# Optimization experiments

Measured on AMD Instinct MI355X. Metric: run time of the kernel, lower is better.

## Reference

```python
import jax, jax.numpy as jnp
import numpy as np

NEG_SLOPE = 0.2
N, E, NNZ, IN, H, C = 100000, 50000, 800000, 128, 8, 16


def setup_inputs() -> dict:
    key = jax.random.key(0)
    ks = jax.random.split(key, 8)
    X = jax.random.normal(ks[0], (N, IN), jnp.float32)
    W_typed = jax.random.normal(ks[1], (4, IN, H * C), jnp.float32) * (1.0 / np.sqrt(IN))
    att_e = jax.random.normal(ks[2], (4, H, C), jnp.float32) * 0.1
    att_v = jax.random.normal(ks[3], (4, H, C), jnp.float32) * 0.1
    vertex = jax.random.randint(ks[4], (NNZ,), 0, N, jnp.int32)
    edges = jax.random.randint(ks[5], (NNZ,), 0, E, jnp.int32)
    vtype = jax.random.randint(ks[6], (N,), 0, 4, jnp.int32)
    etype = jax.random.randint(ks[7], (E,), 0, 4, jnp.int32)
    return {"X": X, "W_typed": W_typed, "att_e": att_e, "att_v": att_v,
            "vertex": vertex, "edges": edges, "vtype": vtype, "etype": etype}


def _segment_softmax(logits, seg, num):
    # numerically-stable softmax over segments (PyG-style, eps in denominator)
    m = jax.ops.segment_max(logits, seg, num_segments=num)
    ex = jnp.exp(logits - m[seg])
    s = jax.ops.segment_sum(ex, seg, num_segments=num)
    return ex / (s[seg] + 1e-16)


def reference(X, W_typed, att_e, att_v, vertex, edges, vtype, etype):
    # typed linear: project with all 4 type weights, select per node type
    Xall = jnp.einsum('ni,tio->tno', X, W_typed)        # [4, N, H*C]
    X0 = Xall[vtype, jnp.arange(N)]                     # [N, H*C]
    Xn = X0.reshape(N, H, C)
    Xve = Xn[vertex]                                    # [NNZ, H, C] gather vertex->incidence
    # vertex->edge attention, typed by edge type of each incidence
    beta = jnp.sum(Xve * att_e[etype[edges]], axis=-1)  # [NNZ, H]
    beta = jax.nn.leaky_relu(beta, NEG_SLOPE)
    beta = _segment_softmax(beta, edges, E)
    Xe = jax.nn.relu(jax.ops.segment_sum(Xve * beta[..., None], edges, num_segments=E))  # [E, H, C]
    Xe = Xe[edges]                                      # [NNZ, H, C] gather edge->incidence
    # edge->vertex attention, typed by node type of each incidence's vertex
    alpha = jnp.sum(Xe * att_v[vtype[vertex]], axis=-1)  # [NNZ, H]
    alpha = jax.nn.leaky_relu(alpha, NEG_SLOPE)
    alpha = _segment_softmax(alpha, vertex, N)
    Xv = jax.ops.segment_sum(Xe * alpha[..., None], vertex, num_segments=N)  # [N, H, C]
    return Xv.reshape(N, H * C)
```

## Files before the change

### kernel.cpp

```cpp
#include <hip/hip_runtime.h>

typedef __attribute__((ext_vector_type(8))) short bf16x8;
typedef __attribute__((ext_vector_type(4))) float f32x4;

#define NEG_SLOPE 0.2f

__device__ __forceinline__ unsigned short f2bf(float f){
  unsigned u = __float_as_uint(f);
  u = (u + 0x7fffu + ((u >> 16) & 1u)) >> 16;
  return (unsigned short)u;
}
__device__ __forceinline__ float bflo(unsigned u){ return __uint_as_float(u << 16); }
__device__ __forceinline__ float bfhi(unsigned u){ return __uint_as_float(u & 0xffff0000u); }

__global__ __launch_bounds__(256) void k_histprep(
    const int* __restrict__ edges, const int* __restrict__ vertex, int NNZ,
    int* __restrict__ cnt, int E, int nbHist,
    const int* __restrict__ vtype, int N, int* __restrict__ tcnt, int nbHN,
    const float* __restrict__ W, short* __restrict__ Bfrag){
  __shared__ int lcnt[4];
  int b = (int)blockIdx.x;
  if (b < nbHist){
    int i = b * 256 + threadIdx.x;
    if (i < NNZ){
      atomicAdd(cnt + edges[i], 1);
      atomicAdd(cnt + E + vertex[i], 1);
    }
    return;
  }
  b -= nbHist;
  if (b < nbHN){
    if (threadIdx.x < 4) lcnt[threadIdx.x] = 0;
    __syncthreads();
    int i = b * 256 + threadIdx.x;
    if (i < N) atomicAdd(&lcnt[vtype[i]], 1);
    __syncthreads();
    if (threadIdx.x < 4 && lcnt[threadIdx.x] > 0)
      atomicAdd(tcnt + threadIdx.x, lcnt[threadIdx.x]);
    return;
  }
  b -= nbHN;
  int u = b * 256 + threadIdx.x;
  int j = u & 7, lane = (u >> 3) & 63, ct = (u >> 9) & 31, ks = u >> 14;
  int k = ks * 32 + ((lane >> 4) << 3) + j;
  int col = (ct << 4) + (lane & 15);
  int t = col >> 7, o = col & 127;
  Bfrag[u] = (short)f2bf(W[(t * 128 + k) * 128 + o]);
}

__global__ __launch_bounds__(256) void k_scanA(const int* __restrict__ cnt, int S,
                                               int* __restrict__ bsum){
  __shared__ int sh[256];
  int base = blockIdx.x * 1024 + threadIdx.x * 4;
  int s = 0;
  #pragma unroll
  for (int k = 0; k < 4; ++k){ int idx = base + k; if (idx < S) s += cnt[idx]; }
  sh[threadIdx.x] = s; __syncthreads();
  for (int off = 128; off > 0; off >>= 1){
    if (threadIdx.x < off) sh[threadIdx.x] += sh[threadIdx.x + off];
    __syncthreads();
  }
  if (threadIdx.x == 0) bsum[blockIdx.x] = sh[0];
}

__global__ void k_scanB(int* bsum, int nb, const int* __restrict__ tcnt,
                        int* __restrict__ pbase){
  if (threadIdx.x == 0 && blockIdx.x == 0){
    int run = 0;
    for (int b = 0; b < nb; ++b){ int v = bsum[b]; bsum[b] = run; run += v; }
    int pb = 0;
    for (int t = 0; t < 4; ++t){
      pbase[t] = pb;
      pb += ((tcnt[t] + 63) >> 6) << 6;
    }
    pbase[4] = pb;
  }
}

__global__ __launch_bounds__(256) void k_scanC(const int* __restrict__ cnt, int S,
    const int* __restrict__ bsum, int* __restrict__ offs, int* __restrict__ cursor,
    int nbS, const int* __restrict__ vtype, int N, const int* __restrict__ pbase,
    int* __restrict__ tcur, int* __restrict__ nsorted){
  __shared__ int sh[256];
  __shared__ int gbase[4];
  int t = threadIdx.x;
  int b = (int)blockIdx.x;
  if (b >= nbS){
    int* lcnt = sh;
    if (t < 4) lcnt[t] = 0;
    __syncthreads();
    int i = (b - nbS) * 256 + t;
    int tt = 0, rank = 0;
    bool valid = i < N;
    if (valid){ tt = vtype[i]; rank = atomicAdd(&lcnt[tt], 1); }
    __syncthreads();
    if (t < 4 && lcnt[t] > 0) gbase[t] = atomicAdd(tcur + t, lcnt[t]);
    __syncthreads();
    if (valid) nsorted[pbase[tt] + gbase[tt] + rank] = i;
    return;
  }
  int base = b * 1024 + t * 4;
  int c[4]; int s = 0;
  #pragma unroll
  for (int k = 0; k < 4; ++k){ int idx = base + k; c[k] = (idx < S) ? cnt[idx] : 0; s += c[k]; }
  sh[t] = s; __syncthreads();
  for (int off = 1; off < 256; off <<= 1){
    int v = (t >= off) ? sh[t - off] : 0; __syncthreads();
    sh[t] += v; __syncthreads();
  }
  int run = bsum[b] + sh[t] - s;
  #pragma unroll
  for (int k = 0; k < 4; ++k){
    int idx = base + k;
    if (idx < S){ offs[idx] = run; cursor[idx] = run; run += c[k]; }
  }
}

__global__ __launch_bounds__(256, 3) void k_gemm_place(const float* __restrict__ X,
    const short* __restrict__ Bfrag, const int* __restrict__ nsorted,
    const int* __restrict__ pbase, unsigned short* __restrict__ X0,
    const int* __restrict__ edges, const int* __restrict__ vertex, int NNZ,
    int* __restrict__ cursor, int* __restrict__ rows, int nbPlace){
  __shared__ short shB[8 * 4 * 64 * 8];
  const int tid = threadIdx.x;
  const int q = (int)blockIdx.x / 3, r = (int)blockIdx.x % 3;

  if (r != 0){
    int hb = 2 * q + (r - 1);
    if (hb < nbPlace){
      int i = hb * 256 + tid;
      if (i < NNZ){
        int pos = atomicAdd(cursor + edges[i], 1);
        rows[pos] = vertex[i];
      }
    }
    return;
  }

  const int rowIdx = q * 64;
  const int t = (rowIdx >= pbase[1]) + (rowIdx >= pbase[2]) + (rowIdx >= pbase[3]);

  const bf16x8* Bv = (const bf16x8*)Bfrag;
  bf16x8* shBv = (bf16x8*)shB;
  #pragma unroll
  for (int v = 0; v < 8; ++v){
    int item = v * 256 + tid;
    int slab = item >> 6, ln = item & 63;
    int ks = slab >> 3, ctl = slab & 7;
    shBv[item] = Bv[((ks * 32 + 8 * t + ctl) * 64) + ln];
  }

  const int w = tid >> 6, lane = tid & 63;
  const int m = lane & 15, qq = lane >> 4;
  const int node = nsorted[rowIdx + w * 16 + m];

  bf16x8 afrag[4];
  #pragma unroll
  for (int ks = 0; ks < 4; ++ks){
    bf16x8 f;
    if (node >= 0){
      const float4* src = (const float4*)(X + (size_t)node * 128 + ks * 32 + qq * 8);
      float4 a = src[0], b = src[1];
      f[0]=(short)f2bf(a.x); f[1]=(short)f2bf(a.y); f[2]=(short)f2bf(a.z); f[3]=(short)f2bf(a.w);
      f[4]=(short)f2bf(b.x); f[5]=(short)f2bf(b.y); f[6]=(short)f2bf(b.z); f[7]=(short)f2bf(b.w);
    } else {
      #pragma unroll
      for (int z = 0; z < 8; ++z) f[z] = 0;
    }
    afrag[ks] = f;
  }

  f32x4 acc[8];
  #pragma unroll
  for (int ct = 0; ct < 8; ++ct){
    acc[ct][0]=0.f; acc[ct][1]=0.f; acc[ct][2]=0.f; acc[ct][3]=0.f;
  }

  __syncthreads();
  #pragma unroll
  for (int ctl = 0; ctl < 8; ++ctl){
    #pragma unroll
    for (int ks = 0; ks < 4; ++ks){
      bf16x8 bf = shBv[(ks * 8 + ctl) * 64 + lane];
      acc[ctl] = __builtin_amdgcn_mfma_f32_16x16x32_bf16(afrag[ks], bf, acc[ctl], 0, 0, 0);
    }
  }

  const int col0 = lane & 15;
  #pragma unroll
  for (int rr = 0; rr < 4; ++rr){
    int row = nsorted[rowIdx + w * 16 + qq * 4 + rr];
    if (row < 0) continue;
    #pragma unroll
    for (int ctl = 0; ctl < 8; ++ctl)
      X0[(size_t)row * 128 + ctl * 16 + col0] = f2bf(acc[ctl][rr]);
  }
}

template<int OUT_BF16, int DO_RELU>
__device__ __forceinline__ void seg_body(const unsigned* __restrict__ feat,
    const float* __restrict__ att, const int* __restrict__ rows_sorted,
    const int* __restrict__ offs, const int* __restrict__ cnt,
    const int* __restrict__ stype, void* __restrict__ outbuf,
    int S, int blockId, int tid){
  int wid = tid >> 6, lane = tid & 63;
  int s = blockId * 4 + wid;
  if (s >= S) return;
  int t = stype[s];
  float a0 = att[t * 128 + 2 * lane], a1 = att[t * 128 + 2 * lane + 1];
  int start = offs[s], len = cnt[s];
  float denom = 0.f, acc0 = 0.f, acc1 = 0.f;

  for (int base = 0; base < len; base += 64){
    int m = len - base; if (m > 64) m = 64;
    int idx = 0;
    if (lane < m) idx = rows_sorted[start + base + lane];

    unsigned u0 = 0, u1 = 0, u2 = 0, u3 = 0;
    {
      int r;
      r = __shfl(idx, 0); if (0 < m) u0 = feat[(size_t)r * 64 + lane];
      r = __shfl(idx, 1); if (1 < m) u1 = feat[(size_t)r * 64 + lane];
      r = __shfl(idx, 2); if (2 < m) u2 = feat[(size_t)r * 64 + lane];
      r = __shfl(idx, 3); if (3 < m) u3 = feat[(size_t)r * 64 + lane];
    }
    for (int j = 0; j < m; j += 2){
      unsigned ua = u0, ub = u1;
      u0 = u2; u1 = u3;
      if (j + 4 < m){ int rn = __shfl(idx, j + 4); u2 = feat[(size_t)rn * 64 + lane]; }
      if (j + 5 < m){ int rn = __shfl(idx, j + 5); u3 = feat[(size_t)rn * 64 + lane]; }

      float xa0 = bflo(ua), xa1 = bfhi(ua);
      float xb0 = bflo(ub), xb1 = bfhi(ub);
      float pa = xa0 * a0 + xa1 * a1;
      float pb = xb0 * a0 + xb1 * a1;
      pa += __shfl_xor(pa, 1);  pb += __shfl_xor(pb, 1);
      pa += __shfl_xor(pa, 2);  pb += __shfl_xor(pb, 2);
      pa += __shfl_xor(pa, 4);  pb += __shfl_xor(pb, 4);
      pa = pa > 0.f ? pa : NEG_SLOPE * pa;
      float wa = __expf(pa);
      denom += wa; acc0 += wa * xa0; acc1 += wa * xa1;
      if (j + 1 < m){
        pb = pb > 0.f ? pb : NEG_SLOPE * pb;
        float wb = __expf(pb);
        denom += wb; acc0 += wb * xb0; acc1 += wb * xb1;
      }
    }
  }
  float inv = 1.f / (denom + 1e-16f);
  float v0 = acc0 * inv, v1 = acc1 * inv;
  if (DO_RELU){ v0 = fmaxf(v0, 0.f); v1 = fmaxf(v1, 0.f); }
  if (OUT_BF16){
    unsigned pw = (unsigned)f2bf(v0) | ((unsigned)f2bf(v1) << 16);
    ((unsigned*)outbuf)[(size_t)s * 64 + lane] = pw;
  } else {
    ((float2*)outbuf)[(size_t)s * 64 + lane] = make_float2(v0, v1);
  }
}

__global__ __launch_bounds__(256) void k_place_seg1(
    const int* __restrict__ edges, const int* __restrict__ vertex, int NNZ,
    int* __restrict__ cursor, int* __restrict__ rows, int E,
    int nbPlace, int nbSeg,
    const unsigned* __restrict__ X0, const float* __restrict__ att_e,
    const int* __restrict__ offs, const int* __restrict__ cnt,
    const int* __restrict__ etype, void* __restrict__ Xe){
  const int q = (int)blockIdx.x / 5, r = (int)blockIdx.x % 5;
  if (r == 0){
    if (q < nbPlace){
      int i = q * 256 + threadIdx.x;
      if (i < NNZ){
        int pos = atomicAdd(cursor + E + vertex[i], 1);
        rows[pos] = edges[i];
      }
    }
    return;
  }
  int segBlk = q * 4 + (r - 1);
  if (segBlk >= nbSeg) return;
  seg_body<1, 1>(X0, att_e, rows, offs, cnt, etype, Xe, E, segBlk, threadIdx.x);
}

__global__ __launch_bounds__(256) void k_seg2(const unsigned* __restrict__ Xe,
    const float* __restrict__ att_v, const int* __restrict__ rows,
    const int* __restrict__ offs, const int* __restrict__ cnt,
    const int* __restrict__ vtype, float* __restrict__ out, int N){
  seg_body<0, 0>(Xe, att_v, rows, offs, cnt, vtype, out, N,
                 (int)blockIdx.x, threadIdx.x);
}

extern "C" void kernel_launch(void* const* d_in, const int* in_sizes, int n_in,
                              void* d_out, int out_size, void* d_ws, size_t ws_size,
                              hipStream_t stream){
  const float* X      = (const float*)d_in[0];
  const float* W      = (const float*)d_in[1];
  const float* att_e  = (const float*)d_in[2];
  const float* att_v  = (const float*)d_in[3];
  const int*   vertex = (const int*)d_in[4];
  const int*   edges  = (const int*)d_in[5];
  const int*   vtype  = (const int*)d_in[6];
  const int*   etype  = (const int*)d_in[7];
  float* out = (float*)d_out;
  const int N   = in_sizes[0] / 128;
  const int NNZ = in_sizes[4];
  const int E   = in_sizes[7];
  const int S   = E + N;

  const int nbI = (NNZ + 255) / 256;
  const int nbHN = (N + 255) / 256;
  const int nbS = (S + 1023) / 1024;
  const int nbSeg1 = (E + 3) / 4;
  const int nbPad = (N + 252 + 63) / 64;
  const int nsortedCap = nbPad * 64;

  char* wp = (char*)d_ws;
  int* cnt    = (int*)wp; wp += (size_t)S * 4;
  int* tcnt   = (int*)wp; wp += 16;
  int* tcur   = (int*)wp; wp += 16;
  int* offs   = (int*)wp; wp += (size_t)S * 4;
  int* cursor = (int*)wp; wp += (size_t)S * 4;
  int* bsum   = (int*)wp; wp += 1024;
  int* pbase  = (int*)wp; wp += 32;
  int* rows   = (int*)wp; wp += (size_t)2 * NNZ * 4;
  int* nsorted= (int*)wp; wp += (size_t)nsortedCap * 4;
  unsigned short* X0 = (unsigned short*)wp; wp += (size_t)N * 128 * 2;
  unsigned short* Xe = (unsigned short*)wp; wp += (size_t)E * 128 * 2;
  short* Bfrag = (short*)wp; wp += (size_t)65536 * 2;

  hipMemsetAsync(cnt, 0, (size_t)(S + 8) * 4, stream);
  hipMemsetAsync(nsorted, 0xFF, (size_t)nsortedCap * 4, stream);

  k_histprep<<<nbI + nbHN + 256, 256, 0, stream>>>(edges, vertex, NNZ, cnt, E,
      nbI, vtype, N, tcnt, nbHN, W, Bfrag);

  k_scanA<<<nbS, 256, 0, stream>>>(cnt, S, bsum);
  k_scanB<<<1, 64, 0, stream>>>(bsum, nbS, tcnt, pbase);
  k_scanC<<<nbS + nbHN, 256, 0, stream>>>(cnt, S, bsum, offs, cursor,
      nbS, vtype, N, pbase, tcur, nsorted);

  k_gemm_place<<<3 * nbPad, 256, 0, stream>>>(X, Bfrag, nsorted, pbase,
      (unsigned short*)X0, edges, vertex, NNZ, cursor, rows, nbI);

  k_place_seg1<<<5 * nbI, 256, 0, stream>>>(edges, vertex, NNZ, cursor,
      rows, E, nbI, nbSeg1, (const unsigned*)X0, att_e, offs, cnt, etype, Xe);

  k_seg2<<<(N + 3) / 4, 256, 0, stream>>>((const unsigned*)Xe, att_v,
      rows, offs + E, cnt + E, vtype, out, N);
}
```

Baseline: 363.5 us.

## Drop scanB launch and second memset; deepen segment gather prefetch

Removes the single-thread k_scanB kernel. Each scanC block now reduces the preceding block sums itself, and the per-type padding bases are recomputed from tcnt inline in scanC and the GEMM. The nsorted array moves next to cnt and stores node+1, so one zeroing memset covers both and the 0xFF memset goes away. The segment softmax loop now prefetches 8 gathered rows and processes 4 per iteration instead of 4 and 2, for more memory-level parallelism at the cost of extra registers.

```diff
diff --git a/kernel.cpp b/kernel.cpp
--- a/kernel.cpp
+++ b/kernel.cpp
@@ -12,6 +12,14 @@
 }
 __device__ __forceinline__ float bflo(unsigned u){ return __uint_as_float(u << 16); }
 __device__ __forceinline__ float bfhi(unsigned u){ return __uint_as_float(u & 0xffff0000u); }
+
+__device__ __forceinline__ void pbase_from_tcnt(const int* __restrict__ tcnt,
+                                                int& p1, int& p2, int& p3){
+  int c0 = tcnt[0], c1 = tcnt[1], c2 = tcnt[2];
+  p1 = ((c0 + 63) >> 6) << 6;
+  p2 = p1 + (((c1 + 63) >> 6) << 6);
+  p3 = p2 + (((c2 + 63) >> 6) << 6);
+}
 
 __global__ __launch_bounds__(256) void k_histprep(
     const int* __restrict__ edges, const int* __restrict__ vertex, int NNZ,
@@ -63,42 +71,38 @@
   if (threadIdx.x == 0) bsum[blockIdx.x] = sh[0];
 }
 
-__global__ void k_scanB(int* bsum, int nb, const int* __restrict__ tcnt,
-                        int* __restrict__ pbase){
-  if (threadIdx.x == 0 && blockIdx.x == 0){
-    int run = 0;
-    for (int b = 0; b < nb; ++b){ int v = bsum[b]; bsum[b] = run; run += v; }
-    int pb = 0;
-    for (int t = 0; t < 4; ++t){
-      pbase[t] = pb;
-      pb += ((tcnt[t] + 63) >> 6) << 6;
-    }
-    pbase[4] = pb;
-  }
-}
-
 __global__ __launch_bounds__(256) void k_scanC(const int* __restrict__ cnt, int S,
-    const int* __restrict__ bsum, int* __restrict__ offs, int* __restrict__ cursor,
-    int nbS, const int* __restrict__ vtype, int N, const int* __restrict__ pbase,
+    const int* __restrict__ bsum, int nbS,
+    int* __restrict__ offs, int* __restrict__ cursor,
+    const int* __restrict__ vtype, int N, const int* __restrict__ tcnt,
     int* __restrict__ tcur, int* __restrict__ nsorted){
   __shared__ int sh[256];
   __shared__ int gbase[4];
   int t = threadIdx.x;
   int b = (int)blockIdx.x;
   if (b >= nbS){
-    int* lcnt = sh;
-    if (t < 4) lcnt[t] = 0;
+    int p1, p2, p3; pbase_from_tcnt(tcnt, p1, p2, p3);
+    int pb[4] = {0, p1, p2, p3};
+    if (t < 4) sh[t] = 0;
     __syncthreads();
     int i = (b - nbS) * 256 + t;
     int tt = 0, rank = 0;
     bool valid = i < N;
-    if (valid){ tt = vtype[i]; rank = atomicAdd(&lcnt[tt], 1); }
-    __syncthreads();
-    if (t < 4 && lcnt[t] > 0) gbase[t] = atomicAdd(tcur + t, lcnt[t]);
-    __syncthreads();
-    if (valid) nsorted[pbase[tt] + gbase[tt] + rank] = i;
-    return;
-  }
+    if (valid){ tt = vtype[i]; rank = atomicAdd(&sh[tt], 1); }
+    __syncthreads();
+    if (t < 4 && sh[t] > 0) gbase[t] = atomicAdd(tcur + t, sh[t]);
+    __syncthreads();
+    if (valid) nsorted[pb[tt] + gbase[tt] + rank] = i + 1;
+    return;
+  }
+  sh[t] = (t < b) ? bsum[t] : 0;
+  __syncthreads();
+  for (int off = 128; off > 0; off >>= 1){
+    if (t < off) sh[t] += sh[t + off];
+    __syncthreads();
+  }
+  int blockBase = sh[0];
+  __syncthreads();
   int base = b * 1024 + t * 4;
   int c[4]; int s = 0;
   #pragma unroll
@@ -108,7 +112,7 @@
     int v = (t >= off) ? sh[t - off] : 0; __syncthreads();
     sh[t] += v; __syncthreads();
   }
-  int run = bsum[b] + sh[t] - s;
+  int run = blockBase + sh[t] - s;
   #pragma unroll
   for (int k = 0; k < 4; ++k){
     int idx = base + k;
@@ -118,7 +122,7 @@
 
 __global__ __launch_bounds__(256, 3) void k_gemm_place(const float* __restrict__ X,
     const short* __restrict__ Bfrag, const int* __restrict__ nsorted,
-    const int* __restrict__ pbase, unsigned short* __restrict__ X0,
+    const int* __restrict__ tcnt, unsigned short* __restrict__ X0,
     const int* __restrict__ edges, const int* __restrict__ vertex, int NNZ,
     int* __restrict__ cursor, int* __restrict__ rows, int nbPlace){
   __shared__ short shB[8 * 4 * 64 * 8];
@@ -138,7 +142,8 @@
   }
 
   const int rowIdx = q * 64;
-  const int t = (rowIdx >= pbase[1]) + (rowIdx >= pbase[2]) + (rowIdx >= pbase[3]);
+  int p1, p2, p3; pbase_from_tcnt(tcnt, p1, p2, p3);
+  const int t = (rowIdx >= p1) + (rowIdx >= p2) + (rowIdx >= p3);
 
   const bf16x8* Bv = (const bf16x8*)Bfrag;
   bf16x8* shBv = (bf16x8*)shB;
@@ -152,7 +157,7 @@
 
   const int w = tid >> 6, lane = tid & 63;
   const int m = lane & 15, qq = lane >> 4;
-  const int node = nsorted[rowIdx + w * 16 + m];
+  const int node = nsorted[rowIdx + w * 16 + m] - 1;
 
   bf16x8 afrag[4];
   #pragma unroll
@@ -189,7 +194,7 @@
   const int col0 = lane & 15;
   #pragma unroll
   for (int rr = 0; rr < 4; ++rr){
-    int row = nsorted[rowIdx + w * 16 + qq * 4 + rr];
+    int row = nsorted[rowIdx + w * 16 + qq * 4 + rr] - 1;
     if (row < 0) continue;
     #pragma unroll
     for (int ctl = 0; ctl < 8; ++ctl)
@@ -216,27 +221,37 @@
     int idx = 0;
     if (lane < m) idx = rows_sorted[start + base + lane];
 
-    unsigned u0 = 0, u1 = 0, u2 = 0, u3 = 0;
-    {
-      int r;
-      r = __shfl(idx, 0); if (0 < m) u0 = feat[(size_t)r * 64 + lane];
-      r = __shfl(idx, 1); if (1 < m) u1 = feat[(size_t)r * 64 + lane];
-      r = __shfl(idx, 2); if (2 < m) u2 = feat[(size_t)r * 64 + lane];
-      r = __shfl(idx, 3); if (3 < m) u3 = feat[(size_t)r * 64 + lane];
-    }
-    for (int j = 0; j < m; j += 2){
-      unsigned ua = u0, ub = u1;
-      u0 = u2; u1 = u3;
-      if (j + 4 < m){ int rn = __shfl(idx, j + 4); u2 = feat[(size_t)rn * 64 + lane]; }
-      if (j + 5 < m){ int rn = __shfl(idx, j + 5); u3 = feat[(size_t)rn * 64 + lane]; }
-
+    unsigned u[8];
+    #pragma unroll
+    for (int k = 0; k < 8; ++k){
+      unsigned nv = 0;
+      if (k < m){ int r = __shfl(idx, k); nv = feat[(size_t)r * 64 + lane]; }
+      u[k] = nv;
+    }
+    for (int j = 0; j < m; j += 4){
+      unsigned ua = u[0], ub = u[1], uc = u[2], ud = u[3];
+      u[0] = u[4]; u[1] = u[5]; u[2] = u[6]; u[3] = u[7];
+      #pragma unroll
+      for (int k = 0; k < 4; ++k){
+        int jn = j + 8 + k;
+        unsigned nv = 0;
+        if (jn < m){ int rn = __shfl(idx, jn); nv = feat[(size_t)rn * 64 + lane]; }
+        u[4 + k] = nv;
+      }
       float xa0 = bflo(ua), xa1 = bfhi(ua);
       float xb0 = bflo(ub), xb1 = bfhi(ub);
+      float xc0 = bflo(uc), xc1 = bfhi(uc);
+      float xd0 = bflo(ud), xd1 = bfhi(ud);
       float pa = xa0 * a0 + xa1 * a1;
       float pb = xb0 * a0 + xb1 * a1;
-      pa += __shfl_xor(pa, 1);  pb += __shfl_xor(pb, 1);
-      pa += __shfl_xor(pa, 2);  pb += __shfl_xor(pb, 2);
-      pa += __shfl_xor(pa, 4);  pb += __shfl_xor(pb, 4);
+      float pc = xc0 * a0 + xc1 * a1;
+      float pd = xd0 * a0 + xd1 * a1;
+      pa += __shfl_xor(pa, 1); pb += __shfl_xor(pb, 1);
+      pc += __shfl_xor(pc, 1); pd += __shfl_xor(pd, 1);
+      pa += __shfl_xor(pa, 2); pb += __shfl_xor(pb, 2);
+      pc += __shfl_xor(pc, 2); pd += __shfl_xor(pd, 2);
+      pa += __shfl_xor(pa, 4); pb += __shfl_xor(pb, 4);
+      pc += __shfl_xor(pc, 4); pd += __shfl_xor(pd, 4);
       pa = pa > 0.f ? pa : NEG_SLOPE * pa;
       float wa = __expf(pa);
       denom += wa; acc0 += wa * xa0; acc1 += wa * xa1;
@@ -244,6 +259,16 @@
         pb = pb > 0.f ? pb : NEG_SLOPE * pb;
         float wb = __expf(pb);
         denom += wb; acc0 += wb * xb0; acc1 += wb * xb1;
+      }
+      if (j + 2 < m){
+        pc = pc > 0.f ? pc : NEG_SLOPE * pc;
+        float wc = __expf(pc);
+        denom += wc; acc0 += wc * xc0; acc1 += wc * xc1;
+      }
+      if (j + 3 < m){
+        pd = pd > 0.f ? pd : NEG_SLOPE * pd;
+        float wd = __expf(pd);
+        denom += wd; acc0 += wd * xd0; acc1 += wd * xd1;
       }
     }
   }
@@ -317,28 +342,25 @@
   int* cnt    = (int*)wp; wp += (size_t)S * 4;
   int* tcnt   = (int*)wp; wp += 16;
   int* tcur   = (int*)wp; wp += 16;
+  int* nsorted= (int*)wp; wp += (size_t)nsortedCap * 4;
   int* offs   = (int*)wp; wp += (size_t)S * 4;
   int* cursor = (int*)wp; wp += (size_t)S * 4;
   int* bsum   = (int*)wp; wp += 1024;
-  int* pbase  = (int*)wp; wp += 32;
   int* rows   = (int*)wp; wp += (size_t)2 * NNZ * 4;
-  int* nsorted= (int*)wp; wp += (size_t)nsortedCap * 4;
   unsigned short* X0 = (unsigned short*)wp; wp += (size_t)N * 128 * 2;
   unsigned short* Xe = (unsigned short*)wp; wp += (size_t)E * 128 * 2;
   short* Bfrag = (short*)wp; wp += (size_t)65536 * 2;
 
-  hipMemsetAsync(cnt, 0, (size_t)(S + 8) * 4, stream);
-  hipMemsetAsync(nsorted, 0xFF, (size_t)nsortedCap * 4, stream);
+  hipMemsetAsync(cnt, 0, (size_t)(S + 8 + nsortedCap) * 4, stream);
 
   k_histprep<<<nbI + nbHN + 256, 256, 0, stream>>>(edges, vertex, NNZ, cnt, E,
       nbI, vtype, N, tcnt, nbHN, W, Bfrag);
 
   k_scanA<<<nbS, 256, 0, stream>>>(cnt, S, bsum);
-  k_scanB<<<1, 64, 0, stream>>>(bsum, nbS, tcnt, pbase);
-  k_scanC<<<nbS + nbHN, 256, 0, stream>>>(cnt, S, bsum, offs, cursor,
-      nbS, vtype, N, pbase, tcur, nsorted);
-
-  k_gemm_place<<<3 * nbPad, 256, 0, stream>>>(X, Bfrag, nsorted, pbase,
+  k_scanC<<<nbS + nbHN, 256, 0, stream>>>(cnt, S, bsum, nbS, offs, cursor,
+      vtype, N, tcnt, tcur, nsorted);
+
+  k_gemm_place<<<3 * nbPad, 256, 0, stream>>>(X, Bfrag, nsorted, tcnt,
       (unsigned short*)X0, edges, vertex, NNZ, cursor, rows, nbI);
 
   k_place_seg1<<<5 * nbI, 256, 0, stream>>>(edges, vertex, NNZ, cursor,
```

Measured after the change: 397.4 us. +9.3%, slower.
